# Optimization experiments

Hardware: AMD Instinct MI355X
Metric: run time of the kernel (lower is better)

## Reference

```python
import jax, jax.numpy as jnp
import numpy as np

B, C1, C2, H, W = 4, 256, 256, 64, 64
K, S, P, D = 3, 1, 1, 1
KK = K * K
BN_EPS = 1e-5
MAX_OFF = float(K * D * 2)


def setup_inputs() -> dict:
    key = jax.random.key(0)
    ks = jax.random.split(key, 8)
    x = jax.random.normal(ks[0], (B, C1, H, W), jnp.float32)
    # offset/mask 3x3 conv (module zero-inits; small random values exercise bilinear sampling)
    w_om = jax.random.normal(ks[1], (3 * KK, C1, 3, 3), jnp.float32) * 0.01
    b_om = jax.random.normal(ks[2], (3 * KK,), jnp.float32) * 0.01
    # main DCN weight [C2, C1, K, K], Kaiming-ish scale
    w_dcn = jax.random.normal(ks[3], (C2, C1, K, K), jnp.float32) * np.float32(1.0 / np.sqrt(C1 * KK))
    bn_gamma = 1.0 + 0.1 * jax.random.normal(ks[4], (C2,), jnp.float32)
    bn_beta = 0.1 * jax.random.normal(ks[5], (C2,), jnp.float32)
    bn_mean = 0.1 * jax.random.normal(ks[6], (C2,), jnp.float32)
    bn_var = jax.random.uniform(ks[7], (C2,), jnp.float32, minval=0.5, maxval=1.5)
    return {"x": x, "w_om": w_om, "b_om": b_om, "w_dcn": w_dcn,
            "bn_gamma": bn_gamma, "bn_beta": bn_beta, "bn_mean": bn_mean, "bn_var": bn_var}


def _dcn_v2(x, w_om, b_om, w_dcn):
    # 1) offset/mask conv (3x3, stride S, 'same' pad)
    om = jax.lax.conv_general_dilated(
        x, w_om, window_strides=(S, S), padding=((1, 1), (1, 1)),
        dimension_numbers=("NCHW", "OIHW", "NCHW")) + b_om[None, :, None, None]
    Ho, Wo = om.shape[2], om.shape[3]
    # 2) clamp offsets, sigmoid mask (mmcv layout: per kernel pos [dy, dx] interleaved)
    off = jnp.clip(om[:, :2 * KK], -MAX_OFF, MAX_OFF).reshape(B, KK, 2, Ho, Wo)
    mask = jax.nn.sigmoid(om[:, 2 * KK:3 * KK])  # [B, KK, Ho, Wo]
    # 3) sampling positions: p = (h*S - P + i*D + dy, w*S - P + j*D + dx)
    ky, kx = jnp.meshgrid(jnp.arange(K), jnp.arange(K), indexing="ij")
    base_y = (ky.reshape(KK) * D)[:, None, None] + (jnp.arange(Ho) * S - P)[None, :, None]  # [KK,Ho,1]
    base_x = (kx.reshape(KK) * D)[:, None, None] + (jnp.arange(Wo) * S - P)[None, None, :]  # [KK,1,Wo]
    py = base_y.astype(x.dtype)[None] + off[:, :, 0]  # [B,KK,Ho,Wo]
    px = base_x.astype(x.dtype)[None] + off[:, :, 1]
    # 4) bilinear gather with zero outside boundaries (per-corner validity, mmcv semantics)
    y0 = jnp.floor(py); x0 = jnp.floor(px)
    ly = py - y0; lx = px - x0
    y0i = y0.astype(jnp.int32); x0i = x0.astype(jnp.int32)
    x_flat = x.reshape(B, C1, H * W)

    def gather(yi, xi):
        valid = ((yi >= 0) & (yi < H) & (xi >= 0) & (xi < W)).astype(x.dtype)
        idx = (jnp.clip(yi, 0, H - 1) * W + jnp.clip(xi, 0, W - 1)).reshape(B, 1, -1)
        g = jnp.take_along_axis(x_flat, idx, axis=2)
        return g.reshape(B, C1, KK, Ho, Wo), valid  # valid: [B,KK,Ho,Wo]

    v00, m00 = gather(y0i, x0i)
    v01, m01 = gather(y0i, x0i + 1)
    v10, m10 = gather(y0i + 1, x0i)
    v11, m11 = gather(y0i + 1, x0i + 1)
    w00 = ((1 - ly) * (1 - lx) * m00)[:, None]
    w01 = ((1 - ly) * lx * m01)[:, None]
    w10 = (ly * (1 - lx) * m10)[:, None]
    w11 = (ly * lx * m11)[:, None]
    col = (w00 * v00 + w01 * v01 + w10 * v10 + w11 * v11) * mask[:, None]  # [B,C1,KK,Ho,Wo]
    # 5) gather-conv accumulate: out[b,o,h,w] = sum_{c,k} W[o,c,k] * col[b,c,k,h,w]
    return jnp.einsum("ock,bckhw->bohw", w_dcn.reshape(C2, C1, KK), col)


def reference(x, w_om, b_om, w_dcn, bn_gamma, bn_beta, bn_mean, bn_var):
    out = _dcn_v2(x, w_om, b_om, w_dcn)
    inv = bn_gamma * jax.lax.rsqrt(bn_var + BN_EPS)
    out = out * inv[None, :, None, None] + (bn_beta - bn_mean * inv)[None, :, None, None]
    return jax.nn.silu(out)
```

## Files before the change

kernel.cpp:

```cpp
#include <hip/hip_runtime.h>
#include <math.h>

#define B_  4
#define C1_ 256
#define C2_ 256
#define H_  64
#define W_  64
#define HW_ 4096
#define KK_ 9

#define A_WA     0u
#define A_XT     1179648u
#define A_XPAIR  9568256u
#define A_MIDX   26345472u
#define A_MWGT   27525120u
#define A_WOM    29884416u
#define A_BN     30031872u

typedef short bf16x8 __attribute__((ext_vector_type(8)));
typedef float f32x4 __attribute__((ext_vector_type(4)));

__device__ __forceinline__ unsigned f2bfu(float f) {
  unsigned u = __builtin_bit_cast(unsigned, f);
  return (u + 0x7FFFu + ((u >> 16) & 1u)) >> 16;
}
__device__ __forceinline__ float bflo(unsigned g) {
  return __builtin_bit_cast(float, g << 16);
}
__device__ __forceinline__ float bfhi(unsigned g) {
  return __builtin_bit_cast(float, g & 0xFFFF0000u);
}
__device__ __forceinline__ void gload_lds16(const void* g, void* l) {
  __builtin_amdgcn_global_load_lds(
      (const __attribute__((address_space(1))) unsigned*)g,
      (__attribute__((address_space(3))) unsigned*)l, 16, 0, 0);
}

__device__ __forceinline__ void decode_bid512(int bid, int& b, int& h, int& ph) {
  const int xcd = bid & 7, slot = bid >> 3;
  b = xcd >> 1;
  h = (xcd & 1) * 32 + (slot >> 1);
  ph = slot & 1;
}

__global__ __launch_bounds__(256) void prep(
    const float* __restrict__ x, const float* __restrict__ w_om,
    const float* __restrict__ w_dcn, const float* __restrict__ bn_gamma,
    const float* __restrict__ bn_beta, const float* __restrict__ bn_mean,
    const float* __restrict__ bn_var, unsigned short* __restrict__ xT,
    unsigned* __restrict__ xpair, unsigned short* __restrict__ Wa,
    unsigned short* __restrict__ Wom, float* __restrict__ bnbuf) {
  const int bid = blockIdx.x;
  const int tid = threadIdx.x;
  if (bid < 1024) {
    __shared__ unsigned short T[64][68];
    const int b = bid >> 8;
    const int rem = bid & 255;
    const int pos0 = (rem >> 2) * 64;
    const int c0 = (rem & 3) * 64;
    const int pl = tid & 63;
    const int ch = tid >> 6;
#pragma unroll
    for (int r = 0; r < 16; ++r) {
      const int cl = ch * 16 + r;
      const float v = x[((size_t)(b * C1_ + c0 + cl)) * HW_ + pos0 + pl];
      T[cl][pl] = (unsigned short)f2bfu(v);
    }
    if (tid < 64) {
      const int pe = min(pos0 + 64, HW_ - 1);
      T[tid][64] =
          (unsigned short)f2bfu(x[((size_t)(b * C1_ + c0 + tid)) * HW_ + pe]);
    }
    __syncthreads();
    unsigned short* dstT = xT + ((size_t)b * HW_ + pos0) * 256 + c0;
#pragma unroll
    for (int it = 0; it < 2; ++it) {
      const int q = it * 256 + tid;
      const int pp = q >> 3, cc = (q & 7) * 8;
      unsigned t0 = T[cc + 0][pp], t1 = T[cc + 1][pp], t2 = T[cc + 2][pp],
               t3 = T[cc + 3][pp], t4 = T[cc + 4][pp], t5 = T[cc + 5][pp],
               t6 = T[cc + 6][pp], t7 = T[cc + 7][pp];
      *(int4*)(dstT + (size_t)pp * 256 + cc) =
          make_int4(t0 | (t1 << 16), t2 | (t3 << 16), t4 | (t5 << 16),
                    t6 | (t7 << 16));
    }
    unsigned* dstP = xpair + ((size_t)b * HW_ + pos0) * 256 + c0;
#pragma unroll
    for (int it = 0; it < 4; ++it) {
      const int q = it * 256 + tid;
      const int pp = q >> 4;
      const int cc = (q & 15) * 4;
      unsigned p0 = (unsigned)T[cc + 0][pp] | ((unsigned)T[cc + 0][pp + 1] << 16);
      unsigned p1 = (unsigned)T[cc + 1][pp] | ((unsigned)T[cc + 1][pp + 1] << 16);
      unsigned p2 = (unsigned)T[cc + 2][pp] | ((unsigned)T[cc + 2][pp + 1] << 16);
      unsigned p3 = (unsigned)T[cc + 3][pp] | ((unsigned)T[cc + 3][pp + 1] << 16);
      *(uint4*)(dstP + (size_t)pp * 256 + cc) = make_uint4(p0, p1, p2, p3);
    }
  } else if (bid < 1024 + 2304) {
    const unsigned e = (bid - 1024) * 256 + tid;
    const unsigned kt = e >> 13, r2 = e & 8191;
    const unsigned kg = r2 >> 11, r3 = r2 & 2047, o = r3 >> 3, j = r3 & 7;
    const unsigned ck = kt * 32 + kg * 8 + j;
    const unsigned k = ck >> 8, c = ck & 255;
    Wa[e] = (unsigned short)f2bfu(w_dcn[((size_t)o * C1_ + c) * 9 + k]);
  } else {
    const int wb = bid - (1024 + 2304);
    if (wb == 0) {
      const int o = tid;
      float inv = bn_gamma[o] * rsqrtf(bn_var[o] + 1e-5f);
      bnbuf[o] = inv;
      bnbuf[256 + o] = bn_beta[o] - bn_mean[o] * inv;
    }
    const unsigned e = wb * 256 + tid;
    const unsigned kt = e >> 10, kg = (e >> 8) & 3, o = (e >> 3) & 31, j = e & 7;
    const unsigned ck = kt * 32 + kg * 8 + j;
    const unsigned k = ck >> 8, c = ck & 255;
    const float v = (o < 27) ? w_om[((size_t)o * C1_ + c) * 9 + k] : 0.f;
    Wom[e] = (unsigned short)f2bfu(v);
  }
}

__global__ __launch_bounds__(256) void om_gemm(
    const unsigned short* __restrict__ xT, const float* __restrict__ b_om,
    const unsigned short* __restrict__ Wom, int2* __restrict__ midx,
    float4* __restrict__ mwgt) {
  __shared__ short Ald[2][4096];
  __shared__ short Bld[2][4096];
  __shared__ float omld[32][33];

  int b, h, ph;
  decode_bid512(blockIdx.x, b, h, ph);
  const int tid = threadIdx.x;
  const int lane = tid & 63, wid = tid >> 6;
  const int wo = wid >> 1, wp = wid & 1;
  const int p = tid & 31;
  const int cr = tid >> 5;

  const unsigned short* xTb = xT + (size_t)b * HW_ * 256;

  f32x4 acc = (f32x4){0.f, 0.f, 0.f, 0.f};

  auto stageA = [&](int s, int buf) {
    const char* src = (const char*)(Wom + (size_t)s * 4096);
    gload_lds16(src + tid * 16, (char*)&Ald[buf][0] + tid * 16);
    gload_lds16(src + (256 + tid) * 16, (char*)&Ald[buf][0] + (256 + tid) * 16);
  };

  auto produce = [&](int s, int4& uA, int4& uB) {
    const int k = s >> 1;
    const int c0 = (s & 1) * 128 + cr * 16;
    const int hh = h - 1 + k / 3;
    const int ww = ph * 32 + p - 1 + k % 3;
    const bool v = ((unsigned)hh < (unsigned)H_) && ((unsigned)ww < (unsigned)W_);
    const unsigned short* pl = xTb + (size_t)(v ? hh * W_ + ww : 0) * 256 + c0;
    uA = v ? *(const int4*)pl : make_int4(0, 0, 0, 0);
    uB = v ? *(const int4*)(pl + 8) : make_int4(0, 0, 0, 0);
  };

  const int bslot = (cr * 2) * 256 + p * 8;

  auto compute = [&](int buf) {
    const int kg = lane >> 4, rr = lane & 15;
#pragma unroll
    for (int kh = 0; kh < 4; ++kh) {
      bf16x8 af = *(const bf16x8*)&Ald[buf][(kh * 4 + kg) * 256 + (wo * 16 + rr) * 8];
      bf16x8 bfr = *(const bf16x8*)&Bld[buf][(kh * 4 + kg) * 256 + (wp * 16 + rr) * 8];
      acc = __builtin_amdgcn_mfma_f32_16x16x32_bf16(af, bfr, acc, 0, 0, 0);
    }
  };

  {
    int4 uA, uB;
    produce(0, uA, uB);
    *(int4*)&Bld[0][bslot] = uA;
    *(int4*)&Bld[0][bslot + 256] = uB;
    stageA(0, 0);
  }
  __syncthreads();

  for (int s = 0; s < 18; ++s) {
    const int cur = s & 1, nxt = cur ^ 1;
    const bool pre = (s < 17);
    int4 uA, uB;
    if (pre) {
      produce(s + 1, uA, uB);
      stageA(s + 1, nxt);
    }
    compute(cur);
    if (pre) {
      *(int4*)&Bld[nxt][bslot] = uA;
      *(int4*)&Bld[nxt][bslot + 256] = uB;
    }
    __syncthreads();
  }

  {
    const int rr = lane & 15, rh = lane >> 4;
#pragma unroll
    for (int r = 0; r < 4; ++r) omld[wo * 16 + rh * 4 + r][wp * 16 + rr] = acc[r];
  }
  __syncthreads();

  if (tid < 32) {
    const int pc = tid;
    float a[27];
#pragma unroll
    for (int oc = 0; oc < 27; ++oc) a[oc] = omld[oc][pc] + b_om[oc];

    const int pcol = ph * 32 + pc;
#pragma unroll
    for (int k = 0; k < 9; ++k) {
      float dy = fminf(fmaxf(a[2 * k], -6.f), 6.f);
      float dx = fminf(fmaxf(a[2 * k + 1], -6.f), 6.f);
      float m = 1.f / (1.f + expf(-a[18 + k]));
      float py = (float)(h - 1 + k / 3) + dy;
      float px = (float)(pcol - 1 + k % 3) + dx;
      float y0f = floorf(py), x0f = floorf(px);
      float ly = py - y0f, lx = px - x0f;
      int y0 = (int)y0f, x0 = (int)x0f;
      int y1 = y0 + 1, x1 = x0 + 1;
      const bool vy0 = ((unsigned)y0 < (unsigned)H_);
      const bool vy1 = ((unsigned)y1 < (unsigned)H_);
      const bool vx0 = ((unsigned)x0 < (unsigned)W_);
      const bool vx1 = ((unsigned)x1 < (unsigned)W_);
      int y0c = min(max(y0, 0), H_ - 1), y1c = min(max(y1, 0), H_ - 1);
      int x0c = min(max(x0, 0), W_ - 1), x1c = min(max(x1, 0), W_ - 1);
      const int xbc = min(max(x0, 0), W_ - 2);
      float wx0 = 0.f, wx1 = 0.f;
      if (vx0) { if (x0c == xbc) wx0 += 1.f - lx; else wx1 += 1.f - lx; }
      if (vx1) { if (x1c == xbc) wx0 += lx; else wx1 += lx; }
      const float wy0 = vy0 ? (1.f - ly) : 0.f;
      const float wy1 = vy1 ? ly : 0.f;
      const size_t e = ((size_t)b * KK_ + k) * HW_ + h * W_ + pcol;
      midx[e] = make_int2(y0c * W_ + xbc, y1c * W_ + xbc);
      mwgt[e] = make_float4(m * wy0 * wx0, m * wy0 * wx1, m * wy1 * wx0,
                            m * wy1 * wx1);
    }
  }
}

__global__ __launch_bounds__(512, 4) void dcn_fused(
    const unsigned short* __restrict__ Wa, const unsigned* __restrict__ xpair,
    const int2* __restrict__ midxg, const float4* __restrict__ mwgtg,
    const float* __restrict__ bnbuf, float* __restrict__ out) {
  __shared__ short Ald[2][16384];
  __shared__ short Bld[2][2048];

  int b, h, ph;
  decode_bid512(blockIdx.x, b, h, ph);
  const int tid = threadIdx.x;
  const int lane = tid & 63, wid = tid >> 6;
  const int pq = tid >> 4;
  const int q = tid & 15;

  const unsigned* xpb = xpair + (size_t)b * HW_ * 256;
  const int pg = h * W_ + ph * 32 + pq;

  int2 miR[9];
  float4 mwR[9];
#pragma unroll
  for (int k = 0; k < 9; ++k) {
    miR[k] = midxg[(size_t)b * KK_ * HW_ + (size_t)k * HW_ + pg];
    mwR[k] = mwgtg[(size_t)b * KK_ * HW_ + (size_t)k * HW_ + pg];
  }

  f32x4 acc[2][2];
#pragma unroll
  for (int i = 0; i < 2; ++i)
#pragma unroll
    for (int j = 0; j < 2; ++j) acc[i][j] = (f32x4){0.f, 0.f, 0.f, 0.f};

  auto stageA = [&](int s, int buf) {
    const char* src = (const char*)(Wa + (size_t)s * 16384);
#pragma unroll
    for (int r = 0; r < 4; ++r) {
      const int chunk = r * 512 + tid;
      gload_lds16(src + chunk * 16, (char*)&Ald[buf][0] + chunk * 16);
    }
  };

  auto issue = [&](int s, uint4& ga, uint4& gb) {
    const int k = s >> 2;
    const int c0 = (s & 3) * 64 + q * 4;
    ga = *(const uint4*)(xpb + (size_t)miR[k].x * 256 + c0);
    gb = *(const uint4*)(xpb + (size_t)miR[k].y * 256 + c0);
  };

  auto pack = [&](int s, const uint4 ga, const uint4 gb, int2& pk) {
    const float4 mw = mwR[s >> 2];
    const unsigned a[4] = {ga.x, ga.y, ga.z, ga.w};
    const unsigned g[4] = {gb.x, gb.y, gb.z, gb.w};
    unsigned bf[4];
#pragma unroll
    for (int i = 0; i < 4; ++i) {
      float v = mw.x * bflo(a[i]) + mw.y * bfhi(a[i]) + mw.z * bflo(g[i]) +
                mw.w * bfhi(g[i]);
      bf[i] = f2bfu(v);
    }
    pk.x = bf[0] | (bf[1] << 16);
    pk.y = bf[2] | (bf[3] << 16);
  };

  const int bslot = (q >> 3) * 1024 + ((q >> 1) & 3) * 256 + pq * 8 + (q & 1) * 4;

  auto compute = [&](int buf) {
    const int kg = lane >> 4, rr = lane & 15;
    bf16x8 af[2][2], bfr[2][2];
#pragma unroll
    for (int kh = 0; kh < 2; ++kh) {
#pragma unroll
      for (int fm = 0; fm < 2; ++fm)
        af[fm][kh] = *(const bf16x8*)&Ald[buf][kh * 8192 + kg * 2048 +
                                              (wid * 32 + fm * 16 + rr) * 8];
#pragma unroll
      for (int fn = 0; fn < 2; ++fn)
        bfr[fn][kh] =
            *(const bf16x8*)&Bld[buf][kh * 1024 + kg * 256 + (fn * 16 + rr) * 8];
    }
#pragma unroll
    for (int kh = 0; kh < 2; ++kh)
#pragma unroll
      for (int fm = 0; fm < 2; ++fm)
#pragma unroll
        for (int fn = 0; fn < 2; ++fn)
          acc[fm][fn] = __builtin_amdgcn_mfma_f32_16x16x32_bf16(
              af[fm][kh], bfr[fn][kh], acc[fm][fn], 0, 0, 0);
  };

  uint4 ga, gb;
  {
    int2 pk;
    issue(0, ga, gb);
    pack(0, ga, gb, pk);
    *(int2*)&Bld[0][bslot] = pk;
    stageA(0, 0);
  }
  __syncthreads();

#pragma unroll
  for (int s = 0; s < 36; ++s) {
    const int cur = s & 1, nxt = cur ^ 1;
    if (s < 35) {
      issue(s + 1, ga, gb);
      stageA(s + 1, nxt);
    }
    compute(cur);
    if (s < 35) {
      int2 pk;
      pack(s + 1, ga, gb, pk);
      *(int2*)&Bld[nxt][bslot] = pk;
    }
    __syncthreads();
  }

  const float* bninv = bnbuf;
  const float* bnbb = bnbuf + 256;
  const int rr = lane & 15, rh = lane >> 4;
#pragma unroll
  for (int fm = 0; fm < 2; ++fm) {
#pragma unroll
    for (int r = 0; r < 4; ++r) {
      const int o = wid * 32 + fm * 16 + rh * 4 + r;
      const float inv = bninv[o], bb = bnbb[o];
#pragma unroll
      for (int fn = 0; fn < 2; ++fn) {
        float t = acc[fm][fn][r] * inv + bb;
        float sv = t / (1.f + expf(-t));
        out[(size_t)(b * C2_ + o) * HW_ + h * W_ + ph * 32 + fn * 16 + rr] = sv;
      }
    }
  }
}

extern "C" void kernel_launch(void* const* d_in, const int* in_sizes, int n_in,
                              void* d_out, int out_size, void* d_ws,
                              size_t ws_size, hipStream_t stream) {
  const float* x = (const float*)d_in[0];
  const float* w_om = (const float*)d_in[1];
  const float* b_om = (const float*)d_in[2];
  const float* w_dcn = (const float*)d_in[3];
  const float* bn_gamma = (const float*)d_in[4];
  const float* bn_beta = (const float*)d_in[5];
  const float* bn_mean = (const float*)d_in[6];
  const float* bn_var = (const float*)d_in[7];
  float* out = (float*)d_out;
  char* wsb = (char*)d_ws;

  unsigned short* Wa = (unsigned short*)(wsb + A_WA);
  unsigned short* xT = (unsigned short*)(wsb + A_XT);
  unsigned* xpair = (unsigned*)(wsb + A_XPAIR);
  int2* midx = (int2*)(wsb + A_MIDX);
  float4* mwgt = (float4*)(wsb + A_MWGT);
  unsigned short* Wom = (unsigned short*)(wsb + A_WOM);
  float* bnbuf = (float*)(wsb + A_BN);

  prep<<<1024 + 2304 + 288, 256, 0, stream>>>(x, w_om, w_dcn, bn_gamma,
                                              bn_beta, bn_mean, bn_var, xT,
                                              xpair, Wa, Wom, bnbuf);
  om_gemm<<<512, 256, 0, stream>>>(xT, b_om, Wom, midx, mwgt);
  dcn_fused<<<512, 512, 0, stream>>>(Wa, xpair, midx, mwgt, bnbuf, out);
}
```

Before: 79.76 us.

## Merge half-row blocks into full-row 1024-thread blocks sharing weight tiles

The main DCN GEMM kernel now uses 256 blocks of 1024 threads, each covering a full output row of 64 pixels, instead of 512 blocks of 512 threads covering half rows. Each staged weight tile in LDS is then reused across twice as many pixel columns, which halves global weight traffic per output. The B tile in LDS gains an XOR swizzle on the column index to reduce bank conflicts on the MFMA operand reads. In exchange the grid has only 256 blocks (about one per CU), and __launch_bounds__(1024,4) may constrain registers and reduce latency hiding.

```diff
diff --git a/kernel.cpp b/kernel.cpp
--- a/kernel.cpp
+++ b/kernel.cpp
@@ -41,6 +41,12 @@
   b = xcd >> 1;
   h = (xcd & 1) * 32 + (slot >> 1);
   ph = slot & 1;
+}
+
+__device__ __forceinline__ void decode_bid256(int bid, int& b, int& h) {
+  const int xcd = bid & 7, slot = bid >> 3;
+  b = xcd >> 1;
+  h = (xcd & 1) * 32 + slot;
 }
 
 __global__ __launch_bounds__(256) void prep(
@@ -239,22 +245,23 @@
   }
 }
 
-__global__ __launch_bounds__(512, 4) void dcn_fused(
+__global__ __launch_bounds__(1024, 4) void dcn_fused(
     const unsigned short* __restrict__ Wa, const unsigned* __restrict__ xpair,
     const int2* __restrict__ midxg, const float4* __restrict__ mwgtg,
     const float* __restrict__ bnbuf, float* __restrict__ out) {
   __shared__ short Ald[2][16384];
-  __shared__ short Bld[2][2048];
-
-  int b, h, ph;
-  decode_bid512(blockIdx.x, b, h, ph);
+  __shared__ short Bld[2][4096];
+
+  int b, h;
+  decode_bid256(blockIdx.x, b, h);
   const int tid = threadIdx.x;
   const int lane = tid & 63, wid = tid >> 6;
-  const int pq = tid >> 4;
+  const int wo = wid >> 1, wp = wid & 1;
+  const int col = tid >> 4;
   const int q = tid & 15;
 
   const unsigned* xpb = xpair + (size_t)b * HW_ * 256;
-  const int pg = h * W_ + ph * 32 + pq;
+  const int pg = h * W_ + col;
 
   int2 miR[9];
   float4 mwR[9];
@@ -273,8 +280,8 @@
   auto stageA = [&](int s, int buf) {
     const char* src = (const char*)(Wa + (size_t)s * 16384);
 #pragma unroll
-    for (int r = 0; r < 4; ++r) {
-      const int chunk = r * 512 + tid;
+    for (int r = 0; r < 2; ++r) {
+      const int chunk = r * 1024 + tid;
       gload_lds16(src + chunk * 16, (char*)&Ald[buf][0] + chunk * 16);
     }
   };
@@ -301,21 +308,25 @@
     pk.y = bf[2] | (bf[3] << 16);
   };
 
-  const int bslot = (q >> 3) * 1024 + ((q >> 1) & 3) * 256 + pq * 8 + (q & 1) * 4;
+  const int wpage = q >> 1;
+  const int wcol = col ^ wpage;
+  const int bslot = (q >> 3) * 2048 + ((q >> 1) & 3) * 512 + wcol * 8 + (q & 1) * 4;
 
   auto compute = [&](int buf) {
     const int kg = lane >> 4, rr = lane & 15;
     bf16x8 af[2][2], bfr[2][2];
 #pragma unroll
     for (int kh = 0; kh < 2; ++kh) {
+      const int page = kh * 4 + kg;
 #pragma unroll
       for (int fm = 0; fm < 2; ++fm)
         af[fm][kh] = *(const bf16x8*)&Ald[buf][kh * 8192 + kg * 2048 +
-                                              (wid * 32 + fm * 16 + rr) * 8];
-#pragma unroll
-      for (int fn = 0; fn < 2; ++fn)
-        bfr[fn][kh] =
-            *(const bf16x8*)&Bld[buf][kh * 1024 + kg * 256 + (fn * 16 + rr) * 8];
+                                              (wo * 32 + fm * 16 + rr) * 8];
+#pragma unroll
+      for (int fn = 0; fn < 2; ++fn) {
+        const int rc = (wp * 32 + fn * 16 + rr) ^ page;
+        bfr[fn][kh] = *(const bf16x8*)&Bld[buf][kh * 2048 + kg * 512 + rc * 8];
+      }
     }
 #pragma unroll
     for (int kh = 0; kh < 2; ++kh)
@@ -360,13 +371,13 @@
   for (int fm = 0; fm < 2; ++fm) {
 #pragma unroll
     for (int r = 0; r < 4; ++r) {
-      const int o = wid * 32 + fm * 16 + rh * 4 + r;
+      const int o = wo * 32 + fm * 16 + rh * 4 + r;
       const float inv = bninv[o], bb = bnbb[o];
 #pragma unroll
       for (int fn = 0; fn < 2; ++fn) {
         float t = acc[fm][fn][r] * inv + bb;
         float sv = t / (1.f + expf(-t));
-        out[(size_t)(b * C2_ + o) * HW_ + h * W_ + ph * 32 + fn * 16 + rr] = sv;
+        out[(size_t)(b * C2_ + o) * HW_ + h * W_ + wp * 32 + fn * 16 + rr] = sv;
       }
     }
   }
@@ -398,5 +409,5 @@
                                               bn_beta, bn_mean, bn_var, xT,
                                               xpair, Wa, Wom, bnbuf);
   om_gemm<<<512, 256, 0, stream>>>(xT, b_om, Wom, midx, mwgt);
-  dcn_fused<<<512, 512, 0, stream>>>(Wa, xpair, midx, mwgt, bnbuf, out);
-}
+  dcn_fused<<<256, 1024, 0, stream>>>(Wa, xpair, midx, mwgt, bnbuf, out);
+}
```

After: 74.98 us. -6.0%, faster.
